# Kernel tuning notes

Measured on AMD Instinct MI355X. Metric: run time of the kernel, lower is better.

The kernel has to match this reference:

```python
import jax, jax.numpy as jnp
import numpy as np

NH = 12          # num attention heads
EPS = 1e-6       # layer-norm eps
B, T_, S_, H, E, IE = 8, 8, 196, 768, 4, 768  # IE = intermediate_size // num_experts


def layernorm(x, g, b):
    m = jnp.mean(x, axis=-1, keepdims=True)
    v = jnp.var(x, axis=-1, keepdims=True)
    return (x - m) / jnp.sqrt(v + EPS) * g + b


def mha(x, qkv_w, qkv_b, proj_w, proj_b):
    # x: [B', N, H]
    Bp, N, Hh = x.shape
    hd = Hh // NH
    qkv = (x @ qkv_w + qkv_b).reshape(Bp, N, 3, NH, hd).transpose(2, 0, 3, 1, 4)
    q, k, v = qkv[0], qkv[1], qkv[2]                      # [B', nh, N, hd]
    attn = jax.nn.softmax(jnp.einsum('bhqd,bhkd->bhqk', q, k) * (hd ** -0.5), axis=-1)
    out = jnp.einsum('bhqk,bhkd->bhqd', attn, v).transpose(0, 2, 1, 3).reshape(Bp, N, Hh)
    return out @ proj_w + proj_b


def moe_mlp(x, gate_up, down, eids):
    # x: [B, N, H]; gate_up: [E, H, 2*IE]; down: [E, IE, H]; eids: [N]
    sel = jax.nn.one_hot(eids, gate_up.shape[0], dtype=x.dtype)  # [N, E]
    gu = jnp.einsum('bnh,ehk,ne->bnk', x, gate_up, sel)          # per-token expert gate+up
    gate, up = gu[..., :IE], gu[..., IE:]
    inter = jax.nn.silu(gate) * up                               # SwiGLU
    return jnp.einsum('bni,eih,ne->bnh', inter, down, sel)


def setup_inputs() -> dict:
    key = jax.random.key(0)
    ks = jax.random.split(key, 16)
    w = lambda k, shp: (jax.random.normal(k, shp, dtype=jnp.float32) * 0.02)
    inp = {
        'x': jax.random.normal(ks[0], (B, T_ * S_, H), dtype=jnp.float32),
        'qkv_w_s': w(ks[1], (H, 3 * H)), 'qkv_b_s': jnp.zeros((3 * H,), jnp.float32),
        'proj_w_s': w(ks[2], (H, H)),    'proj_b_s': jnp.zeros((H,), jnp.float32),
        'qkv_w_t': w(ks[3], (H, 3 * H)), 'qkv_b_t': jnp.zeros((3 * H,), jnp.float32),
        'proj_w_t': w(ks[4], (H, H)),    'proj_b_t': jnp.zeros((H,), jnp.float32),
        'ln_s_g': jnp.ones((H,), jnp.float32), 'ln_s_b': jnp.zeros((H,), jnp.float32),
        'ln_t_g': jnp.ones((H,), jnp.float32), 'ln_t_b': jnp.zeros((H,), jnp.float32),
        'ln_m_g': jnp.ones((H,), jnp.float32), 'ln_m_b': jnp.zeros((H,), jnp.float32),
        'gate_up_proj': w(ks[5], (E, H, 2 * IE)),
        'down_proj': w(ks[6], (E, IE, H)),
        'T': T_, 'S': S_,
        'expert_ids': jax.random.randint(ks[7], (T_ * S_,), 0, E, dtype=jnp.int32),
    }
    return inp


def reference(x, qkv_w_s, qkv_b_s, proj_w_s, proj_b_s,
              qkv_w_t, qkv_b_t, proj_w_t, proj_b_t,
              ln_s_g, ln_s_b, ln_t_g, ln_t_b, ln_m_g, ln_m_b,
              gate_up_proj, down_proj, T, S, expert_ids):
    Bb, N, Hh = x.shape
    # 1) spatial attention over S patches within each of B*T frames
    xs = layernorm(x, ln_s_g, ln_s_b).reshape(Bb * T, S, Hh)
    xs = mha(xs, qkv_w_s, qkv_b_s, proj_w_s, proj_b_s).reshape(Bb, T * S, Hh)
    x = x + xs
    # 2) temporal attention over T frames at each of B*S spatial positions
    xt = layernorm(x, ln_t_g, ln_t_b).reshape(Bb, T, S, Hh).transpose(0, 2, 1, 3).reshape(Bb * S, T, Hh)
    xt = mha(xt, qkv_w_t, qkv_b_t, proj_w_t, proj_b_t)
    xt = xt.reshape(Bb, S, T, Hh).transpose(0, 2, 1, 3).reshape(Bb, T * S, Hh)
    x = x + xt
    # 3) token-routed MoE MLP
    x = x + moe_mlp(layernorm(x, ln_m_g, ln_m_b), gate_up_proj, down_proj, expert_ids)
    return x
```

## Files before the change

### kernel.cpp

```cpp
#include <hip/hip_runtime.h>

typedef __bf16 bf16;
typedef bf16 bf16x8 __attribute__((ext_vector_type(8)));
typedef float f32x4 __attribute__((ext_vector_type(4)));

#define BB 8
#define TT 8
#define SS 196
#define NTOK 1568
#define ROWS 12544
#define HH 768
#define HD 64

__device__ __forceinline__ void gload16(const void* g, void* l) {
  __builtin_amdgcn_global_load_lds(
      (const __attribute__((address_space(1))) void*)g,
      (__attribute__((address_space(3))) void*)l, 16, 0, 0);
}

__global__ __launch_bounds__(256)
void transpose_qkv(const float* __restrict__ in0, const float* __restrict__ in1,
                   bf16* __restrict__ out0, bf16* __restrict__ out1) {
  const int K = 768, N = 2304;
  const float* in = blockIdx.z ? in1 : in0;
  bf16* out = blockIdx.z ? out1 : out0;
  __shared__ float tile[64][65];
  const int k0 = blockIdx.x * 64, n0 = blockIdx.y * 64;
  const int tx = threadIdx.x & 63, ty = threadIdx.x >> 6;
  #pragma unroll
  for (int rr = ty; rr < 64; rr += 4)
    tile[rr][tx] = in[(size_t)(k0 + rr) * N + n0 + tx];
  __syncthreads();
  #pragma unroll
  for (int rr = ty; rr < 64; rr += 4)
    out[(size_t)(n0 + rr) * K + k0 + tx] = (bf16)tile[tx][rr];
}

__global__ __launch_bounds__(256)
void transpose_768(const float* __restrict__ ps, const float* __restrict__ pt,
                   const float* __restrict__ dw,
                   bf16* __restrict__ ops, bf16* __restrict__ opt,
                   bf16* __restrict__ odw) {
  const int K = 768, N = 768;
  const int z = blockIdx.z;
  const float* in;
  bf16* out;
  if (z == 0)      { in = ps; out = ops; }
  else if (z == 1) { in = pt; out = opt; }
  else             { in = dw + (size_t)(z - 2) * K * N; out = odw + (size_t)(z - 2) * K * N; }
  __shared__ float tile[64][65];
  const int k0 = blockIdx.x * 64, n0 = blockIdx.y * 64;
  const int tx = threadIdx.x & 63, ty = threadIdx.x >> 6;
  #pragma unroll
  for (int rr = ty; rr < 64; rr += 4)
    tile[rr][tx] = in[(size_t)(k0 + rr) * N + n0 + tx];
  __syncthreads();
  #pragma unroll
  for (int rr = ty; rr < 64; rr += 4)
    out[(size_t)(n0 + rr) * K + k0 + tx] = (bf16)tile[tx][rr];
}

__global__ __launch_bounds__(256)
void transpose_gu(const float* __restrict__ in, bf16* __restrict__ out) {
  const int K = 768, N = 1536;
  in  += (size_t)blockIdx.z * K * N;
  out += (size_t)blockIdx.z * K * N;
  __shared__ float tile[64][65];
  const int k0 = blockIdx.x * 64, n0 = blockIdx.y * 64;
  const int tx = threadIdx.x & 63, ty = threadIdx.x >> 6;
  const int s = n0 >> 6;
  #pragma unroll
  for (int rr = ty; rr < 64; rr += 4) {
    const int src = (tx < 32) ? (s * 32 + tx) : (768 + s * 32 + tx - 32);
    tile[rr][tx] = in[(size_t)(k0 + rr) * N + src];
  }
  __syncthreads();
  #pragma unroll
  for (int rr = ty; rr < 64; rr += 4)
    out[(size_t)(n0 + rr) * K + k0 + tx] = (bf16)tile[tx][rr];
}

template<typename TI>
__global__ __launch_bounds__(256)
void ln_kernel(const TI* __restrict__ x, const float* __restrict__ g,
               const float* __restrict__ b, bf16* __restrict__ out) {
  const int row = blockIdx.x * 4 + (threadIdx.x >> 6);
  const int lane = threadIdx.x & 63;
  const TI* xr = x + (size_t)row * HH;
  float v[12];
  float sum = 0.f, sq = 0.f;
  #pragma unroll
  for (int i = 0; i < 12; ++i) {
    v[i] = (float)xr[lane + i * 64];
    sum += v[i];
    sq += v[i] * v[i];
  }
  #pragma unroll
  for (int off = 32; off > 0; off >>= 1) {
    sum += __shfl_xor(sum, off);
    sq  += __shfl_xor(sq, off);
  }
  const float mean = sum * (1.f / 768.f);
  const float var = sq * (1.f / 768.f) - mean * mean;
  const float inv = rsqrtf(var + 1e-6f);
  bf16* op = out + (size_t)row * HH;
  #pragma unroll
  for (int i = 0; i < 12; ++i) {
    const int c = lane + i * 64;
    op[c] = (bf16)((v[i] - mean) * inv * g[c] + b[c]);
  }
}

__global__ __launch_bounds__(256)
void ln_moe_kernel(const bf16* __restrict__ x, const float* __restrict__ g,
                   const float* __restrict__ b, const int* __restrict__ invp,
                   bf16* __restrict__ out) {
  const int row = blockIdx.x * 4 + (threadIdx.x >> 6);
  const int lane = threadIdx.x & 63;
  const bf16* xr = x + (size_t)row * HH;
  float v[12];
  float sum = 0.f, sq = 0.f;
  #pragma unroll
  for (int i = 0; i < 12; ++i) {
    v[i] = (float)xr[lane + i * 64];
    sum += v[i];
    sq += v[i] * v[i];
  }
  #pragma unroll
  for (int off = 32; off > 0; off >>= 1) {
    sum += __shfl_xor(sum, off);
    sq  += __shfl_xor(sq, off);
  }
  const float mean = sum * (1.f / 768.f);
  const float var = sq * (1.f / 768.f) - mean * mean;
  const float inv = rsqrtf(var + 1e-6f);
  const int bb = row / NTOK, n = row - bb * NTOK;
  bf16* op = out + ((size_t)invp[n] * 8 + bb) * HH;
  #pragma unroll
  for (int i = 0; i < 12; ++i) {
    const int c = lane + i * 64;
    op[c] = (bf16)((v[i] - mean) * inv * g[c] + b[c]);
  }
}

template<int NF, bool MOE, bool BIAS, bool RESID, bool RB16, bool OBF16,
         bool GUFUSE, bool SCATTER>
__global__ __launch_bounds__(256, 2)
void gemmDP(const bf16* __restrict__ A, const bf16* __restrict__ BT,
            const float* __restrict__ bias, const void* __restrict__ resid,
            float* __restrict__ outF, bf16* __restrict__ outB,
            int N, int K, int NMT,
            const int* __restrict__ perm, const int4* __restrict__ descs,
            const int* __restrict__ meta) {
  constexpr int BUFE = 4096 + NF * 1024;
  __shared__ __align__(16) bf16 lds[3 * BUFE];
  __shared__ int rowLds[128];

  const int tid = threadIdx.x;
  const int G = gridDim.x;
  int work;
  {
    const int q = G >> 3, r = G & 7, xcd = blockIdx.x & 7, pos = blockIdx.x >> 3;
    work = (xcd < r ? xcd * (q + 1) : r * (q + 1) + (xcd - r) * q) + pos;
  }
  int M0 = 0, N0, ncnt = 16;
  if constexpr (MOE) {
    const int ntile = work % NMT, desc = work / NMT;
    if (desc >= meta[0]) return;
    int4 d = descs[desc];
    BT += (size_t)d.x * N * K;
    ncnt = d.z;
    N0 = ntile * (NF * 32);
    M0 = d.y * 8;
    if constexpr (SCATTER) {
      if (tid < 128) {
        const int nl = tid >> 3, b = tid & 7;
        const int n = perm[d.y + (nl < ncnt ? nl : ncnt - 1)];
        rowLds[tid] = b * NTOK + n;
      }
      __syncthreads();
    }
  } else {
    const int mt = work / NMT, nt = work % NMT;
    M0 = mt * 128;
    N0 = nt * (NF * 32);
  }

  const int w = tid >> 6, lane = tid & 63;
  const int wr = w >> 1, wc = w & 1;
  const int lr = lane & 15, lg = lane >> 4;

  const int r0 = tid >> 2;
  const int sseg = ((tid & 3) ^ ((tid >> 3) & 3)) * 8;
  int arow0 = M0 + r0, arow1 = M0 + 64 + r0;
  if constexpr (MOE) {
    arow0 = arow0 < ROWS ? arow0 : ROWS - 1;
    arow1 = arow1 < ROWS ? arow1 : ROWS - 1;
  }
  const bf16* aP0 = A + (size_t)arow0 * K + sseg;
  const bf16* aP1 = A + (size_t)arow1 * K + sseg;
  const bf16* bP[NF / 2];
  #pragma unroll
  for (int i = 0; i < NF / 2; ++i)
    bP[i] = BT + (size_t)(N0 + i * 64 + r0) * K + sseg;

  auto STG = [&](int kt) {
    bf16* buf = lds + (kt % 3) * BUFE;
    const int ko = kt << 5;
    gload16(aP0 + ko, buf + tid * 8);
    gload16(aP1 + ko, buf + 2048 + tid * 8);
    #pragma unroll
    for (int i = 0; i < NF / 2; ++i)
      gload16(bP[i] + ko, buf + 4096 + i * 2048 + tid * 8);
  };

  const int axr = (lg ^ ((lr >> 1) & 3)) * 8;

  f32x4 acc[4][NF] = {};
  const int NT = K >> 5;

  STG(0); STG(1);

  for (int t = 0; t < NT; ++t) {
    if (t + 1 < NT) {
      if constexpr (NF == 8) { asm volatile("s_waitcnt vmcnt(6)" ::: "memory"); }
      else                   { asm volatile("s_waitcnt vmcnt(4)" ::: "memory"); }
    } else {
      asm volatile("s_waitcnt vmcnt(0)" ::: "memory");
    }
    __builtin_amdgcn_s_barrier();
    asm volatile("" ::: "memory");

    const bf16* Ab = lds + (t % 3) * BUFE;
    const bf16* Bb = Ab + 4096;
    bf16x8 a[4], b[NF];
    #pragma unroll
    for (int mf = 0; mf < 4; ++mf) {
      const int row = wr * 64 + mf * 16 + lr;
      a[mf] = *(const bf16x8*)(Ab + row * 32 + axr);
    }
    #pragma unroll
    for (int nf = 0; nf < NF; ++nf) {
      const int row = wc * (NF * 16) + nf * 16 + lr;
      b[nf] = *(const bf16x8*)(Bb + row * 32 + axr);
    }
    if (t + 2 < NT) STG(t + 2);

    __builtin_amdgcn_s_setprio(1);
    #pragma unroll
    for (int mf = 0; mf < 4; ++mf)
      #pragma unroll
      for (int nf = 0; nf < NF; ++nf)
        acc[mf][nf] = __builtin_amdgcn_mfma_f32_16x16x32_bf16(a[mf], b[nf], acc[mf][nf], 0, 0, 0);
    __builtin_amdgcn_s_setprio(0);
    asm volatile("" ::: "memory");
  }

  #pragma unroll
  for (int m = 0; m < 4; ++m) {
    #pragma unroll
    for (int j = 0; j < 4; ++j) {
      const int r = wr * 64 + m * 16 + lg * 4 + j;
      if (MOE && ((r >> 3) >= ncnt)) continue;
      size_t grow;
      if constexpr (MOE && SCATTER) grow = (size_t)rowLds[r];
      else                          grow = (size_t)(M0 + r);
      if constexpr (GUFUSE) {
        const size_t rbase = grow * 768;
        #pragma unroll
        for (int n = 0; n < NF; ++n) {
          if ((n & 3) >= 2) continue;
          const int stripe = (N0 >> 6) + wc * (NF / 4) + (n >> 2);
          const int icol = stripe * 32 + (n & 3) * 16 + lr;
          const float g = acc[m][n][j], u = acc[m][n + 2][j];
          outB[rbase + icol] = (bf16)(g / (1.f + __expf(-g)) * u);
        }
      } else {
        const size_t rbase = grow * N;
        #pragma unroll
        for (int n = 0; n < NF; ++n) {
          const int gcol = N0 + wc * (NF * 16) + n * 16 + lr;
          float v = acc[m][n][j];
          if constexpr (BIAS)  v += bias[gcol];
          if constexpr (RESID) {
            if constexpr (RB16) v += (float)((const bf16*)resid)[rbase + gcol];
            else                v += ((const float*)resid)[rbase + gcol];
          }
          if constexpr (OBF16) outB[rbase + gcol] = (bf16)v;
          else                 outF[rbase + gcol] = v;
        }
      }
    }
  }
}

#define SPAD 208
#define VST 232
__global__ __launch_bounds__(1024, 1)
void attn_spatial(const bf16* __restrict__ qkv, bf16* __restrict__ out) {
  __shared__ __align__(16) bf16 Ks[SPAD * 64];
  __shared__ __align__(16) bf16 Vt[64 * VST];
  __shared__ __align__(16) bf16 Pb[13][16 * VST];

  const int bp = blockIdx.x, h = blockIdx.y;
  const int tid = threadIdx.x;
  const int w = tid >> 6, lane = tid & 63;
  const int lr = lane & 15, lg = lane >> 4;
  const size_t base = (size_t)bp * SS * 2304 + h * HD;

  for (int cb = w * 64; cb < SPAD * 8; cb += 1024) {
    const int c = cb + lane;
    const int row = c >> 3, seg = c & 7;
    const int srow = row < SS ? row : SS - 1;
    const int sseg = seg ^ (row & 7);
    gload16(qkv + base + (size_t)srow * 2304 + 768 + sseg * 8, Ks + cb * 8);
  }
  for (int t = tid; t < 224 * 8; t += 1024) {
    const int k = t >> 3, dseg = t & 7;
    const int sk = k < SS ? k : SS - 1;
    bf16x8 v = *(const bf16x8*)(qkv + base + (size_t)sk * 2304 + 1536 + dseg * 8);
    #pragma unroll
    for (int i = 0; i < 8; ++i) Vt[(dseg * 8 + i) * VST + k] = v[i];
  }
  if (w < 13) {
    bf16* Pw = Pb[w];
    for (int i = lane; i < 256; i += 64)
      Pw[(i >> 4) * VST + 208 + (i & 15)] = (bf16)0.f;
  }
  __syncthreads();

  for (int t = w; t < 13; t += 16) {
    bf16* Pw = Pb[t];
    const int q0 = t * 16;
    const int qr = q0 + lr;
    const bf16* qp = qkv + base + (size_t)(qr < SS ? qr : SS - 1) * 2304 + lg * 8;
    const bf16x8 af0 = *(const bf16x8*)qp;
    const bf16x8 af1 = *(const bf16x8*)(qp + 32);

    f32x4 sc[13];
    #pragma unroll
    for (int f = 0; f < 13; ++f) sc[f] = (f32x4){0.f, 0.f, 0.f, 0.f};
    #pragma unroll
    for (int f = 0; f < 13; ++f) {
      const int key = f * 16 + lr;
      const bf16x8 bv0 = *(const bf16x8*)&Ks[key * 64 + ((lg) ^ (key & 7)) * 8];
      const bf16x8 bv1 = *(const bf16x8*)&Ks[key * 64 + ((4 + lg) ^ (key & 7)) * 8];
      sc[f] = __builtin_amdgcn_mfma_f32_16x16x32_bf16(af0, bv0, sc[f], 0, 0, 0);
      sc[f] = __builtin_amdgcn_mfma_f32_16x16x32_bf16(af1, bv1, sc[f], 0, 0, 0);
    }
    #pragma unroll
    for (int f = 0; f < 13; ++f)
      #pragma unroll
      for (int j = 0; j < 4; ++j) sc[f][j] *= 0.125f;
    if (192 + lr >= SS)
      #pragma unroll
      for (int j = 0; j < 4; ++j) sc[12][j] = -1e30f;

    float mx[4], ls[4];
    #pragma unroll
    for (int j = 0; j < 4; ++j) {
      float m = sc[0][j];
      #pragma unroll
      for (int f = 1; f < 13; ++f) m = fmaxf(m, sc[f][j]);
      #pragma unroll
      for (int off = 1; off < 16; off <<= 1) m = fmaxf(m, __shfl_xor(m, off));
      mx[j] = m;
    }
    #pragma unroll
    for (int j = 0; j < 4; ++j) ls[j] = 0.f;
    #pragma unroll
    for (int f = 0; f < 13; ++f) {
      #pragma unroll
      for (int j = 0; j < 4; ++j) {
        const float p = __expf(sc[f][j] - mx[j]);
        ls[j] += p;
        Pw[(lg * 4 + j) * VST + f * 16 + lr] = (bf16)p;
      }
    }
    #pragma unroll
    for (int j = 0; j < 4; ++j) {
      #pragma unroll
      for (int off = 1; off < 16; off <<= 1) ls[j] += __shfl_xor(ls[j], off);
      ls[j] = 1.f / ls[j];
    }

    f32x4 oacc[4];
    #pragma unroll
    for (int n = 0; n < 4; ++n) oacc[n] = (f32x4){0.f, 0.f, 0.f, 0.f};
    #pragma unroll
    for (int kb = 0; kb < 7; ++kb) {
      const bf16x8 pa = *(const bf16x8*)&Pw[lr * VST + kb * 32 + lg * 8];
      #pragma unroll
      for (int n = 0; n < 4; ++n) {
        const bf16x8 bv = *(const bf16x8*)&Vt[(n * 16 + lr) * VST + kb * 32 + lg * 8];
        oacc[n] = __builtin_amdgcn_mfma_f32_16x16x32_bf16(pa, bv, oacc[n], 0, 0, 0);
      }
    }
    #pragma unroll
    for (int j = 0; j < 4; ++j) {
      const int row = q0 + lg * 4 + j;
      if (row < SS) {
        bf16* op = out + ((size_t)bp * SS + row) * 768 + h * HD;
        #pragma unroll
        for (int n = 0; n < 4; ++n) op[n * 16 + lr] = (bf16)(oacc[n][j] * ls[j]);
      }
    }
  }
}

__global__ __launch_bounds__(256)
void attn_temporal(const bf16* __restrict__ qkv, bf16* __restrict__ out) {
  const int pair = blockIdx.x * 4 + (threadIdx.x >> 6);
  const int lane = threadIdx.x & 63;
  const int h = pair % 12;
  const int bs = pair / 12;
  const int b = bs / SS, s = bs - b * SS;
  const size_t row0 = (size_t)b * NTOK + s;
  const int q = lane >> 3, k = lane & 7;
  const bf16* qr = qkv + (row0 + (size_t)q * SS) * 2304 + h * HD;
  const bf16* kr = qkv + (row0 + (size_t)k * SS) * 2304 + 768 + h * HD;
  float sc = 0.f;
  #pragma unroll
  for (int j = 0; j < 8; ++j) {
    bf16x8 qv = ((const bf16x8*)qr)[j];
    bf16x8 kv = ((const bf16x8*)kr)[j];
    #pragma unroll
    for (int d = 0; d < 8; ++d) sc += (float)qv[d] * (float)kv[d];
  }
  sc *= 0.125f;
  float mxv = sc;
  #pragma unroll
  for (int off = 1; off < 8; off <<= 1) mxv = fmaxf(mxv, __shfl_xor(mxv, off));
  float p = __expf(sc - mxv);
  float sum = p;
  #pragma unroll
  for (int off = 1; off < 8; off <<= 1) sum += __shfl_xor(sum, off);
  p /= sum;

  const int dg = lane & 7;
  float o[8] = {0, 0, 0, 0, 0, 0, 0, 0};
  #pragma unroll
  for (int kk = 0; kk < 8; ++kk) {
    const float pk = __shfl(p, (lane & 56) + kk);
    const bf16* vr = qkv + (row0 + (size_t)kk * SS) * 2304 + 1536 + h * HD + dg * 8;
    bf16x8 vv = *(const bf16x8*)vr;
    #pragma unroll
    for (int j = 0; j < 8; ++j) o[j] += pk * (float)vv[j];
  }
  bf16* op = out + (row0 + (size_t)q * SS) * 768 + h * HD + dg * 8;
  bf16x8 ov;
  #pragma unroll
  for (int j = 0; j < 8; ++j) ov[j] = (bf16)o[j];
  *(bf16x8*)op = ov;
}

__global__ __launch_bounds__(256)
void sort_moe(const int* __restrict__ eids, int* __restrict__ perm,
              int* __restrict__ invp, int4* __restrict__ descs,
              int* __restrict__ meta) {
  __shared__ int cnt[4], base[4], cur[4];
  const int tid = threadIdx.x;
  if (tid < 4) cnt[tid] = 0;
  __syncthreads();
  for (int n = tid; n < NTOK; n += 256) atomicAdd(&cnt[eids[n]], 1);
  __syncthreads();
  if (tid == 0) {
    int off = 0;
    for (int e = 0; e < 4; ++e) { base[e] = off; cur[e] = off; off += cnt[e]; }
  }
  __syncthreads();
  for (int n = tid; n < NTOK; n += 256) {
    const int pos = atomicAdd(&cur[eids[n]], 1);
    perm[pos] = n;
    invp[n] = pos;
  }
  if (tid == 0) {
    int t = 0;
    for (int e = 0; e < 4; ++e)
      for (int st = 0; st < cnt[e]; st += 16) {
        const int c = cnt[e] - st;
        descs[t++] = make_int4(e, base[e] + st, c < 16 ? c : 16, 0);
      }
    meta[0] = t;
  }
}

extern "C" void kernel_launch(void* const* d_in, const int* in_sizes, int n_in,
                              void* d_out, int out_size, void* d_ws, size_t ws_size,
                              hipStream_t stream) {
  (void)in_sizes; (void)n_in; (void)out_size; (void)ws_size;
  const float* x        = (const float*)d_in[0];
  const float* qkv_w_s  = (const float*)d_in[1];
  const float* qkv_b_s  = (const float*)d_in[2];
  const float* proj_w_s = (const float*)d_in[3];
  const float* proj_b_s = (const float*)d_in[4];
  const float* qkv_w_t  = (const float*)d_in[5];
  const float* qkv_b_t  = (const float*)d_in[6];
  const float* proj_w_t = (const float*)d_in[7];
  const float* proj_b_t = (const float*)d_in[8];
  const float* ln_s_g   = (const float*)d_in[9];
  const float* ln_s_b   = (const float*)d_in[10];
  const float* ln_t_g   = (const float*)d_in[11];
  const float* ln_t_b   = (const float*)d_in[12];
  const float* ln_m_g   = (const float*)d_in[13];
  const float* ln_m_b   = (const float*)d_in[14];
  const float* gate_up  = (const float*)d_in[15];
  const float* down_w   = (const float*)d_in[16];
  const int* expert_ids = (const int*)d_in[19];
  float* out = (float*)d_out;

  char* ws = (char*)d_ws;
  bf16* qkvsT   = (bf16*)(ws + 0);
  bf16* projsT  = (bf16*)(ws + 3538944);
  bf16* qkvtT   = (bf16*)(ws + 4718592);
  bf16* projtT  = (bf16*)(ws + 8257536);
  bf16* guT     = (bf16*)(ws + 9437184);
  bf16* downT   = (bf16*)(ws + 18874368);
  bf16* lnbuf   = (bf16*)(ws + 23592960);
  bf16* qkvbuf  = (bf16*)(ws + 42860544);
  bf16* attnbuf = (bf16*)(ws + 100663296);
  bf16* x1b     = (bf16*)(ws + 119930880);
  bf16* x2b     = (bf16*)(ws + 139198464);
  int*  perm    = (int*)(ws + 158466048);
  int4* descs   = (int4*)(ws + 158472320);
  int*  meta    = (int*)(ws + 158473952);
  int*  invp    = (int*)(ws + 100663296);

  const dim3 blk(256);

  transpose_qkv<<<dim3(12, 36, 2), blk, 0, stream>>>(qkv_w_s, qkv_w_t, qkvsT, qkvtT);
  transpose_768<<<dim3(12, 12, 6), blk, 0, stream>>>(proj_w_s, proj_w_t, down_w,
                                                     projsT, projtT, downT);
  transpose_gu<<<dim3(12, 24, 4), blk, 0, stream>>>(gate_up, guT);

  ln_kernel<float><<<3136, blk, 0, stream>>>(x, ln_s_g, ln_s_b, lnbuf);
  gemmDP<8, false, true, false, false, true, false, false><<<dim3(98 * 9), blk, 0, stream>>>(
      lnbuf, qkvsT, qkv_b_s, nullptr, nullptr, qkvbuf, 2304, 768, 9,
      nullptr, nullptr, nullptr);
  attn_spatial<<<dim3(64, 12), dim3(1024), 0, stream>>>(qkvbuf, attnbuf);
  gemmDP<8, false, true, true, false, true, false, false><<<dim3(98 * 3), blk, 0, stream>>>(
      attnbuf, projsT, proj_b_s, x, nullptr, x1b, 768, 768, 3,
      nullptr, nullptr, nullptr);

  ln_kernel<bf16><<<3136, blk, 0, stream>>>(x1b, ln_t_g, ln_t_b, lnbuf);
  gemmDP<8, false, true, false, false, true, false, false><<<dim3(98 * 9), blk, 0, stream>>>(
      lnbuf, qkvtT, qkv_b_t, nullptr, nullptr, qkvbuf, 2304, 768, 9,
      nullptr, nullptr, nullptr);
  attn_temporal<<<4704, blk, 0, stream>>>(qkvbuf, attnbuf);
  gemmDP<8, false, true, true, true, true, false, false><<<dim3(98 * 3), blk, 0, stream>>>(
      attnbuf, projtT, proj_b_t, x1b, nullptr, x2b, 768, 768, 3,
      nullptr, nullptr, nullptr);

  sort_moe<<<1, blk, 0, stream>>>(expert_ids, perm, invp, descs, meta);
  ln_moe_kernel<<<3136, blk, 0, stream>>>(x2b, ln_m_g, ln_m_b, invp, lnbuf);
  gemmDP<4, true, false, false, false, true, true, false><<<dim3(12 * 102), blk, 0, stream>>>(
      lnbuf, guT, nullptr, nullptr, nullptr, qkvbuf, 1536, 768, 12,
      perm, descs, meta);
  gemmDP<8, true, false, true, true, false, false, true><<<dim3(3 * 102), blk, 0, stream>>>(
      qkvbuf, downT, nullptr, x2b, out, nullptr, 768, 768, 3,
      perm, descs, meta);
}
```

Before: 361.2 us.

## Add 128x128 K64 double-buffered GEMM for QKV projections

Adds a dedicated bf16 MFMA GEMM with 128x128 output tiles, a K step of 64, an XOR-swizzled LDS layout and two-stage global-to-LDS prefetch. It replaces the generic gemmDP kernel for both QKV projections, doubling the tile count (98x18) to improve occupancy and load balance. The new kernel writes the epilogue with scalar stores and handles bias only, so it gives up the generic kernel's wider tiles and possibly vectorized stores.

```diff
diff --git a/kernel.cpp b/kernel.cpp
--- a/kernel.cpp
+++ b/kernel.cpp
@@ -140,6 +140,101 @@
   for (int i = 0; i < 12; ++i) {
     const int c = lane + i * 64;
     op[c] = (bf16)((v[i] - mean) * inv * g[c] + b[c]);
+  }
+}
+
+__global__ __launch_bounds__(256, 2)
+void gemmK64(const bf16* __restrict__ A, const bf16* __restrict__ BT,
+             const float* __restrict__ bias, bf16* __restrict__ outB,
+             int N, int K, int NMT) {
+  __shared__ __align__(16) bf16 lds[2 * 16384];
+  const int tid = threadIdx.x;
+  const int G = gridDim.x;
+  int work;
+  {
+    const int q = G >> 3, r = G & 7, xcd = blockIdx.x & 7, pos = blockIdx.x >> 3;
+    work = (xcd < r ? xcd * (q + 1) : r * (q + 1) + (xcd - r) * q) + pos;
+  }
+  const int mt = work / NMT, nt = work % NMT;
+  const int M0 = mt * 128, N0 = nt * 128;
+
+  const int w = tid >> 6, lane = tid & 63;
+  const int wr = w >> 1, wc = w & 1;
+  const int lr = lane & 15, lg = lane >> 4;
+
+  size_t aG[4], bG[4]; int L[4];
+  #pragma unroll
+  for (int i = 0; i < 4; ++i) {
+    const int c = tid + i * 256;
+    const int row = c >> 3, seg = (c & 7) ^ (row & 7);
+    aG[i] = (size_t)(M0 + row) * K + seg * 8;
+    bG[i] = (size_t)(N0 + row) * K + seg * 8;
+    L[i] = c * 8;
+  }
+  auto STG = [&](int kt) {
+    bf16* buf = lds + (kt & 1) * 16384;
+    const int ko = kt << 6;
+    #pragma unroll
+    for (int i = 0; i < 4; ++i) gload16(A + aG[i] + ko, buf + L[i]);
+    #pragma unroll
+    for (int i = 0; i < 4; ++i) gload16(BT + bG[i] + ko, buf + 8192 + L[i]);
+  };
+
+  f32x4 acc[4][4] = {};
+  const int NT = K >> 6;
+
+  STG(0); STG(1);
+
+  for (int t = 0; t < NT; ++t) {
+    if (t == 0) { asm volatile("s_waitcnt vmcnt(8)" ::: "memory"); }
+    else        { asm volatile("s_waitcnt vmcnt(0)" ::: "memory"); }
+    __builtin_amdgcn_s_barrier();
+    asm volatile("" ::: "memory");
+
+    const bf16* Ab = lds + (t & 1) * 16384;
+    const bf16* Bb = Ab + 8192;
+    bf16x8 a[8], b[8];
+    #pragma unroll
+    for (int mf = 0; mf < 4; ++mf) {
+      const int row = wr * 64 + mf * 16 + lr;
+      #pragma unroll
+      for (int kg = 0; kg < 2; ++kg)
+        a[mf * 2 + kg] = *(const bf16x8*)(Ab + row * 64 + ((kg * 4 + lg) ^ (lr & 7)) * 8);
+    }
+    #pragma unroll
+    for (int nf = 0; nf < 4; ++nf) {
+      const int row = wc * 64 + nf * 16 + lr;
+      #pragma unroll
+      for (int kg = 0; kg < 2; ++kg)
+        b[nf * 2 + kg] = *(const bf16x8*)(Bb + row * 64 + ((kg * 4 + lg) ^ (lr & 7)) * 8);
+    }
+    if (t >= 1 && t + 1 < NT) STG(t + 1);
+
+    __builtin_amdgcn_s_setprio(1);
+    #pragma unroll
+    for (int mf = 0; mf < 4; ++mf)
+      #pragma unroll
+      for (int nf = 0; nf < 4; ++nf) {
+        f32x4 c = acc[mf][nf];
+        c = __builtin_amdgcn_mfma_f32_16x16x32_bf16(a[mf * 2 + 0], b[nf * 2 + 0], c, 0, 0, 0);
+        c = __builtin_amdgcn_mfma_f32_16x16x32_bf16(a[mf * 2 + 1], b[nf * 2 + 1], c, 0, 0, 0);
+        acc[mf][nf] = c;
+      }
+    __builtin_amdgcn_s_setprio(0);
+    asm volatile("" ::: "memory");
+  }
+
+  #pragma unroll
+  for (int m = 0; m < 4; ++m) {
+    #pragma unroll
+    for (int j = 0; j < 4; ++j) {
+      const size_t rbase = (size_t)(M0 + wr * 64 + m * 16 + lg * 4 + j) * N;
+      #pragma unroll
+      for (int n = 0; n < 4; ++n) {
+        const int gcol = N0 + wc * 64 + n * 16 + lr;
+        outB[rbase + gcol] = (bf16)(acc[m][n][j] + bias[gcol]);
+      }
+    }
   }
 }
 
@@ -534,18 +629,16 @@
   transpose_gu<<<dim3(12, 24, 4), blk, 0, stream>>>(gate_up, guT);
 
   ln_kernel<float><<<3136, blk, 0, stream>>>(x, ln_s_g, ln_s_b, lnbuf);
-  gemmDP<8, false, true, false, false, true, false, false><<<dim3(98 * 9), blk, 0, stream>>>(
-      lnbuf, qkvsT, qkv_b_s, nullptr, nullptr, qkvbuf, 2304, 768, 9,
-      nullptr, nullptr, nullptr);
+  gemmK64<<<dim3(98 * 18), blk, 0, stream>>>(
+      lnbuf, qkvsT, qkv_b_s, qkvbuf, 2304, 768, 18);
   attn_spatial<<<dim3(64, 12), dim3(1024), 0, stream>>>(qkvbuf, attnbuf);
   gemmDP<8, false, true, true, false, true, false, false><<<dim3(98 * 3), blk, 0, stream>>>(
       attnbuf, projsT, proj_b_s, x, nullptr, x1b, 768, 768, 3,
       nullptr, nullptr, nullptr);
 
   ln_kernel<bf16><<<3136, blk, 0, stream>>>(x1b, ln_t_g, ln_t_b, lnbuf);
-  gemmDP<8, false, true, false, false, true, false, false><<<dim3(98 * 9), blk, 0, stream>>>(
-      lnbuf, qkvtT, qkv_b_t, nullptr, nullptr, qkvbuf, 2304, 768, 9,
-      nullptr, nullptr, nullptr);
+  gemmK64<<<dim3(98 * 18), blk, 0, stream>>>(
+      lnbuf, qkvtT, qkv_b_t, qkvbuf, 2304, 768, 18);
   attn_temporal<<<4704, blk, 0, stream>>>(qkvbuf, attnbuf);
   gemmDP<8, false, true, true, true, true, false, false><<<dim3(98 * 3), blk, 0, stream>>>(
       attnbuf, projtT, proj_b_t, x1b, nullptr, x2b, 768, 768, 3,
```

Measured after the change: 356.7 us. Within noise of the previous version (-1.3%).
